# Kernel optimization log

Measured on AMD Instinct MI355X. Metric: run time of the kernel, lower is better.

## Reference

```python
import jax, jax.numpy as jnp
import numpy as np

B, T, C, H = 4, 2048, 768, 12
HD = C // H
EPS = 1e-5

def _ln(x, s, b):
    m = jnp.mean(x, axis=-1, keepdims=True)
    v = jnp.mean(jnp.square(x - m), axis=-1, keepdims=True)
    return (x - m) * jax.lax.rsqrt(v + EPS) * s + b

def setup_inputs() -> dict:
    key = jax.random.key(0)
    ks = jax.random.split(key, 8)
    x = jax.random.normal(ks[0], (B, T, C), dtype=jnp.float32)
    mask = jnp.tril(jnp.ones((T, T), dtype=bool))[None, None, :, :]  # causal [1,1,T,T]
    s = lambda fan_in: 1.0 / np.sqrt(fan_in)
    return {
        "x": x,
        "mask": mask,
        "ln1_s": jnp.ones((C,), jnp.float32),
        "ln1_b": jnp.zeros((C,), jnp.float32),
        "w_attn": jax.random.normal(ks[1], (C, 3 * C), jnp.float32) * s(C),
        "b_attn": jnp.zeros((3 * C,), jnp.float32),
        "w_o": jax.random.normal(ks[2], (C, C), jnp.float32) * s(C),
        "b_o": jnp.zeros((C,), jnp.float32),
        "ln2_s": jnp.ones((C,), jnp.float32),
        "ln2_b": jnp.zeros((C,), jnp.float32),
        "w_fc": jax.random.normal(ks[3], (C, 4 * C), jnp.float32) * s(C),
        "b_fc": jnp.zeros((4 * C,), jnp.float32),
        "w_proj": jax.random.normal(ks[4], (4 * C, C), jnp.float32) * s(4 * C),
        "b_proj": jnp.zeros((C,), jnp.float32),
    }

def reference(x, mask, ln1_s, ln1_b, w_attn, b_attn, w_o, b_o,
              ln2_s, ln2_b, w_fc, b_fc, w_proj, b_proj):
    # --- attention branch (pre-LN) ---
    h = _ln(x, ln1_s, ln1_b)
    qkv = (h @ w_attn + b_attn).reshape(B, T, 3 * H, HD)
    q, k, v = jnp.array_split(qkv, 3, axis=2)  # each [B,T,H,HD]
    scale = 1.0 / jnp.sqrt(jnp.float32(HD))
    attn = jnp.einsum('bqhd,bkhd->bhqk', q, k) * scale
    attn = jnp.where(mask, attn, jnp.finfo(jnp.float32).min)
    attn = jax.nn.softmax(attn, axis=-1)
    ctx = jnp.einsum('bhqk,bkhd->bqhd', attn, v).reshape(B, T, C)
    x = x + ctx @ w_o + b_o
    # --- MLP branch (pre-LN) ---
    h = _ln(x, ln2_s, ln2_b)
    h = jax.nn.gelu(h @ w_fc + b_fc, approximate=True)
    x = x + h @ w_proj + b_proj
    return x
```

## Files before the change

### kernel.cpp

```cpp
#include <hip/hip_runtime.h>


typedef unsigned short u16;
typedef unsigned int u32;
typedef __attribute__((ext_vector_type(8))) short short8;
typedef __attribute__((ext_vector_type(4))) float f32x4;
typedef __attribute__((ext_vector_type(16))) float f32x16;

__device__ __forceinline__ u16 f2bf(float f) {
    union { float f; unsigned u; } v; v.f = f;
    unsigned u = v.u;
    unsigned r = (u + 0x7FFFu + ((u >> 16) & 1u)) >> 16;
    return (u16)r;
}

__device__ __forceinline__ u32 cvtpk_bf16(float lo, float hi) {
    u32 r;
    asm("v_cvt_pk_bf16_f32 %0, %1, %2" : "=v"(r) : "v"(lo), "v"(hi));
    return r;
}

__device__ __forceinline__ void gld16(const u16* g, u16* l) {
    __builtin_amdgcn_global_load_lds(
        (const __attribute__((address_space(1))) void*)g,
        (__attribute__((address_space(3))) void*)l, 16, 0, 0);
}

__device__ __forceinline__ float gelu_fast(float v) {
    float t = v * v;
    float z2n = v * (-2.3022078f - 0.10294376f * t);
    float e = __builtin_amdgcn_exp2f(z2n);
    return v * __builtin_amdgcn_rcpf(1.0f + e);
}

__global__ void transpose_all_kernel(const float* __restrict__ w_attn, u16* __restrict__ wT_attn,
                                     const float* __restrict__ w_o,    u16* __restrict__ wT_o,
                                     const float* __restrict__ w_fc,   u16* __restrict__ wT_fc,
                                     const float* __restrict__ w_proj, u16* __restrict__ wT_proj) {
    __shared__ float t[32][33];
    int tile = blockIdx.x;
    const float* w; u16* wt; int N; int idx;
    if (tile < 1728)      { w = w_attn; wt = wT_attn; N = 2304; idx = tile; }
    else if (tile < 2304) { w = w_o;    wt = wT_o;    N = 768;  idx = tile - 1728; }
    else if (tile < 4608) { w = w_fc;   wt = wT_fc;   N = 3072; idx = tile - 2304; }
    else                  { w = w_proj; wt = wT_proj; N = 768;  idx = tile - 4608; }
    int K = (tile >= 4608) ? 3072 : 768;
    int nx = N / 32;
    int n0 = (idx % nx) * 32, k0 = (idx / nx) * 32;
    int tx = threadIdx.x, ty = threadIdx.y;
#pragma unroll
    for (int i = 0; i < 4; i++)
        t[ty + 8 * i][tx] = w[(size_t)(k0 + ty + 8 * i) * N + n0 + tx];
    __syncthreads();
#pragma unroll
    for (int i = 0; i < 4; i++)
        wt[(size_t)(n0 + ty + 8 * i) * K + k0 + tx] = f2bf(t[tx][ty + 8 * i]);
}

__global__ void ln_kernel(const float* __restrict__ x, const float* __restrict__ s,
                          const float* __restrict__ b, u16* __restrict__ out) {
    int row = blockIdx.x;
    int tid = threadIdx.x;
    const float* xr = x + (size_t)row * 768;
    float v0 = xr[tid], v1 = xr[tid + 256], v2 = xr[tid + 512];
    float sum = v0 + v1 + v2;
    float sq = v0 * v0 + v1 * v1 + v2 * v2;
#pragma unroll
    for (int off = 32; off; off >>= 1) {
        sum += __shfl_down(sum, off);
        sq += __shfl_down(sq, off);
    }
    __shared__ float red[8];
    int wid = tid >> 6, lane = tid & 63;
    if (lane == 0) { red[wid] = sum; red[4 + wid] = sq; }
    __syncthreads();
    if (tid == 0) {
        float s4 = red[0] + red[1] + red[2] + red[3];
        float q4 = red[4] + red[5] + red[6] + red[7];
        red[0] = s4 * (1.0f / 768.0f);
        red[1] = q4 * (1.0f / 768.0f);
    }
    __syncthreads();
    float mean = red[0];
    float var = red[1] - mean * mean;
    float rstd = rsqrtf(var + 1e-5f);
    u16* orow = out + (size_t)row * 768;
    orow[tid]       = f2bf((v0 - mean) * rstd * s[tid]       + b[tid]);
    orow[tid + 256] = f2bf((v1 - mean) * rstd * s[tid + 256] + b[tid + 256]);
    orow[tid + 512] = f2bf((v2 - mean) * rstd * s[tid + 512] + b[tid + 512]);
}

template <int GELU, int RES, int OUTMODE, int BM>
__global__ __launch_bounds__(256) void gemm_kernel(
    const u16* __restrict__ A, const u16* __restrict__ Wt,
    const float* __restrict__ bias, const float* __restrict__ res,
    void* __restrict__ out, int M, int N, int K,
    u16* __restrict__ qbuf, u16* __restrict__ kbuf, u16* __restrict__ vbuf) {
    constexpr int FM = BM / 32;
    constexpr int SA = BM / 32;
    constexpr int WR = BM / 2;
    __shared__ __align__(16) u16 lA[2][BM * 64];
    __shared__ __align__(16) u16 lB[2][128 * 64];
    int m0 = blockIdx.x * BM, n0 = blockIdx.y * 128;
    int tid = threadIdx.x;
    int wid = tid >> 6, lane = tid & 63;
    int wr = wid >> 1, wc = wid & 1;
    int l15 = lane & 15, lhi = lane >> 4;

    const u16* aptr[SA];
    const u16* bptr[4];
#pragma unroll
    for (int s = 0; s < SA; s++) {
        int u = s * 256 + tid;
        int row = u >> 3;
        int c8 = (u & 7) ^ (row & 7);
        aptr[s] = A + (size_t)(m0 + row) * K + c8 * 8;
    }
#pragma unroll
    for (int s = 0; s < 4; s++) {
        int u = s * 256 + tid;
        int row = u >> 3;
        int c8 = (u & 7) ^ (row & 7);
        bptr[s] = Wt + (size_t)(n0 + row) * K + c8 * 8;
    }

    f32x4 acc[FM][4];
#pragma unroll
    for (int i = 0; i < FM; i++)
#pragma unroll
        for (int j = 0; j < 4; j++) acc[i][j] = (f32x4)0.0f;

#pragma unroll
    for (int s = 0; s < SA; s++) gld16(aptr[s], &lA[0][(s * 256 + tid) * 8]);
#pragma unroll
    for (int s = 0; s < 4; s++) gld16(bptr[s], &lB[0][(s * 256 + tid) * 8]);
    __syncthreads();

    int KT = K >> 6;
    int cur = 0;
    for (int t = 0; t < KT; t++) {
        if (t + 1 < KT) {
            int ko = (t + 1) << 6;
#pragma unroll
            for (int s = 0; s < SA; s++) gld16(aptr[s] + ko, &lA[cur ^ 1][(s * 256 + tid) * 8]);
#pragma unroll
            for (int s = 0; s < 4; s++) gld16(bptr[s] + ko, &lB[cur ^ 1][(s * 256 + tid) * 8]);
        }
        short8 af[2][FM], bfr[2][4];
#pragma unroll
        for (int ks = 0; ks < 2; ks++) {
#pragma unroll
            for (int f = 0; f < FM; f++) {
                int ra = wr * WR + f * 16 + l15;
                af[ks][f] = *(const short8*)&lA[cur][ra * 64 + (((ks * 4 + lhi) ^ (ra & 7)) << 3)];
            }
#pragma unroll
            for (int f = 0; f < 4; f++) {
                int rb = wc * 64 + f * 16 + l15;
                bfr[ks][f] = *(const short8*)&lB[cur][rb * 64 + (((ks * 4 + lhi) ^ (rb & 7)) << 3)];
            }
        }
#pragma unroll
        for (int ks = 0; ks < 2; ks++)
#pragma unroll
            for (int fm = 0; fm < FM; fm++)
#pragma unroll
                for (int fn = 0; fn < 4; fn++)
                    acc[fm][fn] = __builtin_amdgcn_mfma_f32_16x16x32_bf16(
                        af[ks][fm], bfr[ks][fn], acc[fm][fn], 0, 0, 0);
        __syncthreads();
        cur ^= 1;
    }

    if (OUTMODE == 2) {
        int region = n0 / 768;
#pragma unroll
        for (int fm = 0; fm < FM; fm++)
#pragma unroll
            for (int fn = 0; fn < 4; fn++) {
                int col = n0 + wc * 64 + fn * 16 + l15;
                float bv = bias[col];
                int c = col - region * 768;
                int h = c >> 6, d = c & 63;
#pragma unroll
                for (int r = 0; r < 4; r++) {
                    int row = m0 + wr * WR + fm * 16 + lhi * 4 + r;
                    int bb = row >> 11, t = row & 2047;
                    u16 val = f2bf(acc[fm][fn][r] + bv);
                    size_t bh = (size_t)bb * 12 + h;
                    if (region == 0)      qbuf[(bh * 2048 + t) * 64 + d] = val;
                    else if (region == 1) kbuf[(bh * 2048 + t) * 64 + d] = val;
                    else                  vbuf[(bh * 64 + d) * 2048 + t] = val;
                }
            }
    } else {
#pragma unroll
        for (int fm = 0; fm < FM; fm++)
#pragma unroll
            for (int fn = 0; fn < 4; fn++) {
                int col = n0 + wc * 64 + fn * 16 + l15;
                float bv = bias[col];
#pragma unroll
                for (int r = 0; r < 4; r++) {
                    int row = m0 + wr * WR + fm * 16 + lhi * 4 + r;
                    float v = acc[fm][fn][r] + bv;
                    if (RES) v += res[(size_t)row * N + col];
                    if (GELU) v = gelu_fast(v);
                    if (OUTMODE == 1)
                        ((u16*)out)[(size_t)row * N + col] = f2bf(v);
                    else
                        ((float*)out)[(size_t)row * N + col] = v;
                }
            }
    }
}

__global__ __launch_bounds__(256) void attn_kernel(const u16* __restrict__ qbuf,
                                                   const u16* __restrict__ kbuf,
                                                   const u16* __restrict__ vbuf,
                                                   u16* __restrict__ ctx) {
    int bid = blockIdx.x;
    int qt = 15 - (bid / 48);
    int bh = bid % 48;
    int b = bh / 12, h = bh % 12;
    int q0 = qt * 128;
    int tid = threadIdx.x, wid = tid >> 6, lane = tid & 63;
    int l31 = lane & 31, hi = lane >> 5;

    __shared__ __align__(16) u16 lK[2][64 * 64];
    __shared__ __align__(16) u16 lV[2][64 * 64];

    const size_t bhT = (size_t)bh * 2048;

    const u16* kp[2];
    const u16* vp[2];
#pragma unroll
    for (int s = 0; s < 2; s++) {
        int u = s * 256 + tid;
        int row = u >> 3;
        int c8 = (u & 7) ^ (row & 7);
        kp[s] = kbuf + (bhT + row) * 64 + c8 * 8;
        vp[s] = vbuf + ((size_t)bh * 64 + row) * 2048 + c8 * 8;
    }

    int qrow = q0 + wid * 32 + l31;
    short8 bq[4];
#pragma unroll
    for (int ks = 0; ks < 4; ks++)
        bq[ks] = *(const short8*)(qbuf + (bhT + qrow) * 64 + ks * 16 + hi * 8);

    short8 ones;
#pragma unroll
    for (int j = 0; j < 8; j++) ones[j] = (short)0x3F80;

    f32x16 oacc[2], sacc;
#pragma unroll
    for (int dt = 0; dt < 2; dt++) oacc[dt] = (f32x16)0.0f;
    sacc = (f32x16)0.0f;
    float mb = -1e30f;
    const float C2 = 0.125f * 1.44269504089f;
    const float THR = 11.55f;
    int myq = q0 + wid * 32 + l31;
    int qmax = q0 + wid * 32 + 31;

    int nt = 2 * qt + 2;
#pragma unroll
    for (int s = 0; s < 2; s++) gld16(kp[s], &lK[0][(s * 256 + tid) * 8]);
#pragma unroll
    for (int s = 0; s < 2; s++) gld16(vp[s], &lV[0][(s * 256 + tid) * 8]);
    __syncthreads();

    int cur = 0;
    for (int t = 0; t < nt; t++) {
        int k0 = t * 64;
        if (t + 1 < nt) {
            int kn = (t + 1) * 64;
#pragma unroll
            for (int s = 0; s < 2; s++) gld16(kp[s] + (size_t)kn * 64, &lK[cur ^ 1][(s * 256 + tid) * 8]);
#pragma unroll
            for (int s = 0; s < 2; s++) gld16(vp[s] + kn, &lV[cur ^ 1][(s * 256 + tid) * 8]);
        }
        if (k0 <= qmax) {
            f32x16 sa[2];
#pragma unroll
            for (int kt = 0; kt < 2; kt++) sa[kt] = (f32x16)0.0f;
            __builtin_amdgcn_s_setprio(1);
#pragma unroll
            for (int kt = 0; kt < 2; kt++) {
                int rk = kt * 32 + l31;
#pragma unroll
                for (int ks = 0; ks < 4; ks++) {
                    short8 ak = *(const short8*)&lK[cur][rk * 64 + (((ks * 2 + hi) ^ (rk & 7)) << 3)];
                    sa[kt] = __builtin_amdgcn_mfma_f32_32x32x16_bf16(ak, bq[ks], sa[kt], 0, 0, 0);
                }
            }
            __builtin_amdgcn_s_setprio(0);
            if (k0 + 63 > q0 + wid * 32) {
#pragma unroll
                for (int kt = 0; kt < 2; kt++)
#pragma unroll
                    for (int r = 0; r < 16; r++) {
                        int key = k0 + kt * 32 + (r & 3) + 8 * (r >> 2) + 4 * hi;
                        if (key > myq) sa[kt][r] = -1e30f;
                    }
            }
            float tmax = -1e30f;
#pragma unroll
            for (int kt = 0; kt < 2; kt++)
#pragma unroll
                for (int r = 0; r < 16; r += 2)
                    tmax = fmaxf(tmax, fmaxf(sa[kt][r], sa[kt][r + 1]));
            tmax = fmaxf(tmax, __shfl_xor(tmax, 32));
            float tmb = tmax * C2;
            if (__any(tmb > mb + THR)) {
                float mbn = fmaxf(mb, tmb);
                float corr = __builtin_amdgcn_exp2f(mb - mbn);
#pragma unroll
                for (int r = 0; r < 16; r++) {
                    int qm = (r & 3) + 8 * (r >> 2) + 4 * hi;
                    float c = __shfl(corr, qm);
                    oacc[0][r] *= c;
                    oacc[1][r] *= c;
                    sacc[r] *= c;
                }
                mb = mbn;
            }
#pragma unroll
            for (int kt = 0; kt < 2; kt++)
#pragma unroll
                for (int r = 0; r < 16; r++)
                    sa[kt][r] = __builtin_amdgcn_exp2f(fmaf(sa[kt][r], C2, -mb));
            short8 pa[4];
#pragma unroll
            for (int kt = 0; kt < 2; kt++)
#pragma unroll
                for (int ks2 = 0; ks2 < 2; ks2++) {
                    int base = ks2 * 8;
                    u32 A0 = cvtpk_bf16(sa[kt][base + 0], sa[kt][base + 1]);
                    u32 B0 = cvtpk_bf16(sa[kt][base + 4], sa[kt][base + 5]);
                    u32 A1 = cvtpk_bf16(sa[kt][base + 2], sa[kt][base + 3]);
                    u32 B1 = cvtpk_bf16(sa[kt][base + 6], sa[kt][base + 7]);
                    u32 A0s = (u32)__shfl_xor((int)A0, 32);
                    u32 B0s = (u32)__shfl_xor((int)B0, 32);
                    u32 A1s = (u32)__shfl_xor((int)A1, 32);
                    u32 B1s = (u32)__shfl_xor((int)B1, 32);
                    union { u32 u[4]; short8 s; } w;
                    w.u[0] = hi ? B0s : A0;
                    w.u[1] = hi ? B1s : A1;
                    w.u[2] = hi ? B0 : A0s;
                    w.u[3] = hi ? B1 : A1s;
                    pa[kt * 2 + ks2] = w.s;
                }
            __builtin_amdgcn_s_setprio(1);
#pragma unroll
            for (int kt = 0; kt < 2; kt++)
#pragma unroll
                for (int ks2 = 0; ks2 < 2; ks2++) {
                    short8 ap = pa[kt * 2 + ks2];
#pragma unroll
                    for (int dt = 0; dt < 2; dt++) {
                        int rd = dt * 32 + l31;
                        short8 bv = *(const short8*)&lV[cur][rd * 64 + (((kt * 4 + ks2 * 2 + hi) ^ (rd & 7)) << 3)];
                        oacc[dt] = __builtin_amdgcn_mfma_f32_32x32x16_bf16(ap, bv, oacc[dt], 0, 0, 0);
                    }
                    sacc = __builtin_amdgcn_mfma_f32_32x32x16_bf16(ap, ones, sacc, 0, 0, 0);
                }
            __builtin_amdgcn_s_setprio(0);
        }
        __syncthreads();
        cur ^= 1;
    }
    const size_t rowb = (size_t)b * 2048;
#pragma unroll
    for (int r = 0; r < 16; r++) {
        float ir = __builtin_amdgcn_rcpf(sacc[r]);
        int qm = (r & 3) + 8 * (r >> 2) + 4 * hi;
        int row = q0 + wid * 32 + qm;
        u16* op = ctx + (rowb + row) * 768 + h * 64 + l31;
        op[0]  = f2bf(oacc[0][r] * ir);
        op[32] = f2bf(oacc[1][r] * ir);
    }
}

extern "C" void kernel_launch(void* const* d_in, const int* in_sizes, int n_in,
                              void* d_out, int out_size, void* d_ws, size_t ws_size,
                              hipStream_t stream) {
    const float* x      = (const float*)d_in[0];
    const float* ln1_s  = (const float*)d_in[2];
    const float* ln1_b  = (const float*)d_in[3];
    const float* w_attn = (const float*)d_in[4];
    const float* b_attn = (const float*)d_in[5];
    const float* w_o    = (const float*)d_in[6];
    const float* b_o    = (const float*)d_in[7];
    const float* ln2_s  = (const float*)d_in[8];
    const float* ln2_b  = (const float*)d_in[9];
    const float* w_fc   = (const float*)d_in[10];
    const float* b_fc   = (const float*)d_in[11];
    const float* w_proj = (const float*)d_in[12];
    const float* b_proj = (const float*)d_in[13];

    char* ws = (char*)d_ws;
    u16* wT_attn = (u16*)(ws + 0);
    u16* wT_o    = (u16*)(ws + 3538944);
    u16* wT_fc   = (u16*)(ws + 4718592);
    u16* wT_proj = (u16*)(ws + 9437184);
    u16* bufA    = (u16*)(ws + 14155776);
    u16* qbuf    = (u16*)(ws + 26738688);
    u16* kbuf    = (u16*)(ws + 39321600);
    u16* vbuf    = (u16*)(ws + 51904512);
    u16* act     = (u16*)(ws + 26738688);
    float* x1    = (float*)(ws + 77070336);

    transpose_all_kernel<<<6912, dim3(32, 8), 0, stream>>>(w_attn, wT_attn, w_o, wT_o,
                                                           w_fc, wT_fc, w_proj, wT_proj);

    ln_kernel<<<8192, 256, 0, stream>>>(x, ln1_s, ln1_b, bufA);
    gemm_kernel<0, 0, 2, 128><<<dim3(64, 18), 256, 0, stream>>>(bufA, wT_attn, b_attn, nullptr, nullptr,
                                                                8192, 2304, 768, qbuf, kbuf, vbuf);
    attn_kernel<<<768, 256, 0, stream>>>(qbuf, kbuf, vbuf, bufA);
    gemm_kernel<0, 1, 0, 64><<<dim3(128, 6), 256, 0, stream>>>(bufA, wT_o, b_o, x, x1,
                                                               8192, 768, 768, nullptr, nullptr, nullptr);
    ln_kernel<<<8192, 256, 0, stream>>>(x1, ln2_s, ln2_b, bufA);
    gemm_kernel<1, 0, 1, 128><<<dim3(64, 24), 256, 0, stream>>>(bufA, wT_fc, b_fc, nullptr, act,
                                                                8192, 3072, 768, nullptr, nullptr, nullptr);
    gemm_kernel<0, 1, 0, 64><<<dim3(128, 6), 256, 0, stream>>>(act, wT_proj, b_proj, x1, (float*)d_out,
                                                               8192, 768, 3072, nullptr, nullptr, nullptr);
}
```

Measured before the change: 267.8 us.

## Split GEMM into 256-row big-tile kernel and single-buffered small kernel

```diff
diff --git a/kernel.cpp b/kernel.cpp
--- a/kernel.cpp
+++ b/kernel.cpp
@@ -90,92 +90,73 @@
     orow[tid + 512] = f2bf((v2 - mean) * rstd * s[tid + 512] + b[tid + 512]);
 }
 
-template <int GELU, int RES, int OUTMODE, int BM>
-__global__ __launch_bounds__(256) void gemm_kernel(
+template <int GELU, int OUTMODE>
+__global__ __launch_bounds__(512) void gemm_big_kernel(
     const u16* __restrict__ A, const u16* __restrict__ Wt,
-    const float* __restrict__ bias, const float* __restrict__ res,
-    void* __restrict__ out, int M, int N, int K,
+    const float* __restrict__ bias, void* __restrict__ out,
+    int M, int N, int K,
     u16* __restrict__ qbuf, u16* __restrict__ kbuf, u16* __restrict__ vbuf) {
-    constexpr int FM = BM / 32;
-    constexpr int SA = BM / 32;
-    constexpr int WR = BM / 2;
-    __shared__ __align__(16) u16 lA[2][BM * 64];
-    __shared__ __align__(16) u16 lB[2][128 * 64];
-    int m0 = blockIdx.x * BM, n0 = blockIdx.y * 128;
+    __shared__ __align__(16) u16 lA[256 * 64];
+    __shared__ __align__(16) u16 lB[128 * 64];
+    int m0 = blockIdx.x * 256, n0 = blockIdx.y * 128;
     int tid = threadIdx.x;
     int wid = tid >> 6, lane = tid & 63;
     int wr = wid >> 1, wc = wid & 1;
     int l15 = lane & 15, lhi = lane >> 4;
 
-    const u16* aptr[SA];
-    const u16* bptr[4];
-#pragma unroll
-    for (int s = 0; s < SA; s++) {
-        int u = s * 256 + tid;
+    const u16* aptr[4];
+    const u16* bptr[2];
+#pragma unroll
+    for (int s = 0; s < 4; s++) {
+        int u = s * 512 + tid;
         int row = u >> 3;
         int c8 = (u & 7) ^ (row & 7);
         aptr[s] = A + (size_t)(m0 + row) * K + c8 * 8;
     }
 #pragma unroll
-    for (int s = 0; s < 4; s++) {
-        int u = s * 256 + tid;
+    for (int s = 0; s < 2; s++) {
+        int u = s * 512 + tid;
         int row = u >> 3;
         int c8 = (u & 7) ^ (row & 7);
         bptr[s] = Wt + (size_t)(n0 + row) * K + c8 * 8;
     }
 
-    f32x4 acc[FM][4];
-#pragma unroll
-    for (int i = 0; i < FM; i++)
+    f32x4 acc[4][4];
+#pragma unroll
+    for (int i = 0; i < 4; i++)
 #pragma unroll
         for (int j = 0; j < 4; j++) acc[i][j] = (f32x4)0.0f;
 
-#pragma unroll
-    for (int s = 0; s < SA; s++) gld16(aptr[s], &lA[0][(s * 256 + tid) * 8]);
-#pragma unroll
-    for (int s = 0; s < 4; s++) gld16(bptr[s], &lB[0][(s * 256 + tid) * 8]);
-    __syncthreads();
-
-    int KT = K >> 6;
-    int cur = 0;
-    for (int t = 0; t < KT; t++) {
-        if (t + 1 < KT) {
-            int ko = (t + 1) << 6;
-#pragma unroll
-            for (int s = 0; s < SA; s++) gld16(aptr[s] + ko, &lA[cur ^ 1][(s * 256 + tid) * 8]);
-#pragma unroll
-            for (int s = 0; s < 4; s++) gld16(bptr[s] + ko, &lB[cur ^ 1][(s * 256 + tid) * 8]);
-        }
-        short8 af[2][FM], bfr[2][4];
+    for (int k0 = 0; k0 < K; k0 += 64) {
+#pragma unroll
+        for (int s = 0; s < 4; s++) gld16(aptr[s] + k0, &lA[(s * 512 + tid) * 8]);
+#pragma unroll
+        for (int s = 0; s < 2; s++) gld16(bptr[s] + k0, &lB[(s * 512 + tid) * 8]);
+        __syncthreads();
 #pragma unroll
         for (int ks = 0; ks < 2; ks++) {
-#pragma unroll
-            for (int f = 0; f < FM; f++) {
-                int ra = wr * WR + f * 16 + l15;
-                af[ks][f] = *(const short8*)&lA[cur][ra * 64 + (((ks * 4 + lhi) ^ (ra & 7)) << 3)];
-            }
+            short8 af[4], bfr[4];
 #pragma unroll
             for (int f = 0; f < 4; f++) {
+                int ra = wr * 64 + f * 16 + l15;
+                af[f] = *(const short8*)&lA[ra * 64 + (((ks * 4 + lhi) ^ (ra & 7)) << 3)];
                 int rb = wc * 64 + f * 16 + l15;
-                bfr[ks][f] = *(const short8*)&lB[cur][rb * 64 + (((ks * 4 + lhi) ^ (rb & 7)) << 3)];
-            }
-        }
-#pragma unroll
-        for (int ks = 0; ks < 2; ks++)
-#pragma unroll
-            for (int fm = 0; fm < FM; fm++)
+                bfr[f] = *(const short8*)&lB[rb * 64 + (((ks * 4 + lhi) ^ (rb & 7)) << 3)];
+            }
+#pragma unroll
+            for (int fm = 0; fm < 4; fm++)
 #pragma unroll
                 for (int fn = 0; fn < 4; fn++)
                     acc[fm][fn] = __builtin_amdgcn_mfma_f32_16x16x32_bf16(
-                        af[ks][fm], bfr[ks][fn], acc[fm][fn], 0, 0, 0);
+                        af[fm], bfr[fn], acc[fm][fn], 0, 0, 0);
+        }
         __syncthreads();
-        cur ^= 1;
     }
 
     if (OUTMODE == 2) {
         int region = n0 / 768;
 #pragma unroll
-        for (int fm = 0; fm < FM; fm++)
+        for (int fm = 0; fm < 4; fm++)
 #pragma unroll
             for (int fn = 0; fn < 4; fn++) {
                 int col = n0 + wc * 64 + fn * 16 + l15;
@@ -184,7 +165,7 @@
                 int h = c >> 6, d = c & 63;
 #pragma unroll
                 for (int r = 0; r < 4; r++) {
-                    int row = m0 + wr * WR + fm * 16 + lhi * 4 + r;
+                    int row = m0 + wr * 64 + fm * 16 + lhi * 4 + r;
                     int bb = row >> 11, t = row & 2047;
                     u16 val = f2bf(acc[fm][fn][r] + bv);
                     size_t bh = (size_t)bb * 12 + h;
@@ -195,24 +176,97 @@
             }
     } else {
 #pragma unroll
-        for (int fm = 0; fm < FM; fm++)
+        for (int fm = 0; fm < 4; fm++)
 #pragma unroll
             for (int fn = 0; fn < 4; fn++) {
                 int col = n0 + wc * 64 + fn * 16 + l15;
                 float bv = bias[col];
 #pragma unroll
                 for (int r = 0; r < 4; r++) {
-                    int row = m0 + wr * WR + fm * 16 + lhi * 4 + r;
+                    int row = m0 + wr * 64 + fm * 16 + lhi * 4 + r;
                     float v = acc[fm][fn][r] + bv;
-                    if (RES) v += res[(size_t)row * N + col];
                     if (GELU) v = gelu_fast(v);
-                    if (OUTMODE == 1)
-                        ((u16*)out)[(size_t)row * N + col] = f2bf(v);
-                    else
-                        ((float*)out)[(size_t)row * N + col] = v;
-                }
-            }
-    }
+                    ((u16*)out)[(size_t)row * N + col] = f2bf(v);
+                }
+            }
+    }
+}
+
+__global__ __launch_bounds__(256) void gemm_small_kernel(
+    const u16* __restrict__ A, const u16* __restrict__ Wt,
+    const float* __restrict__ bias, const float* __restrict__ res,
+    float* __restrict__ out, int M, int N, int K) {
+    __shared__ __align__(16) u16 lA[64 * 64];
+    __shared__ __align__(16) u16 lB[128 * 64];
+    int m0 = blockIdx.x * 64, n0 = blockIdx.y * 128;
+    int tid = threadIdx.x;
+    int wid = tid >> 6, lane = tid & 63;
+    int wr = wid >> 1, wc = wid & 1;
+    int l15 = lane & 15, lhi = lane >> 4;
+
+    const u16* aptr[2];
+    const u16* bptr[4];
+#pragma unroll
+    for (int s = 0; s < 2; s++) {
+        int u = s * 256 + tid;
+        int row = u >> 3;
+        int c8 = (u & 7) ^ (row & 7);
+        aptr[s] = A + (size_t)(m0 + row) * K + c8 * 8;
+    }
+#pragma unroll
+    for (int s = 0; s < 4; s++) {
+        int u = s * 256 + tid;
+        int row = u >> 3;
+        int c8 = (u & 7) ^ (row & 7);
+        bptr[s] = Wt + (size_t)(n0 + row) * K + c8 * 8;
+    }
+
+    f32x4 acc[2][4];
+#pragma unroll
+    for (int i = 0; i < 2; i++)
+#pragma unroll
+        for (int j = 0; j < 4; j++) acc[i][j] = (f32x4)0.0f;
+
+    for (int k0 = 0; k0 < K; k0 += 64) {
+#pragma unroll
+        for (int s = 0; s < 2; s++) gld16(aptr[s] + k0, &lA[(s * 256 + tid) * 8]);
+#pragma unroll
+        for (int s = 0; s < 4; s++) gld16(bptr[s] + k0, &lB[(s * 256 + tid) * 8]);
+        __syncthreads();
+#pragma unroll
+        for (int ks = 0; ks < 2; ks++) {
+            short8 af[2], bfr[4];
+#pragma unroll
+            for (int f = 0; f < 2; f++) {
+                int ra = wr * 32 + f * 16 + l15;
+                af[f] = *(const short8*)&lA[ra * 64 + (((ks * 4 + lhi) ^ (ra & 7)) << 3)];
+            }
+#pragma unroll
+            for (int f = 0; f < 4; f++) {
+                int rb = wc * 64 + f * 16 + l15;
+                bfr[f] = *(const short8*)&lB[rb * 64 + (((ks * 4 + lhi) ^ (rb & 7)) << 3)];
+            }
+#pragma unroll
+            for (int fm = 0; fm < 2; fm++)
+#pragma unroll
+                for (int fn = 0; fn < 4; fn++)
+                    acc[fm][fn] = __builtin_amdgcn_mfma_f32_16x16x32_bf16(
+                        af[fm], bfr[fn], acc[fm][fn], 0, 0, 0);
+        }
+        __syncthreads();
+    }
+#pragma unroll
+    for (int fm = 0; fm < 2; fm++)
+#pragma unroll
+        for (int fn = 0; fn < 4; fn++) {
+            int col = n0 + wc * 64 + fn * 16 + l15;
+            float bv = bias[col];
+#pragma unroll
+            for (int r = 0; r < 4; r++) {
+                int row = m0 + wr * 32 + fm * 16 + lhi * 4 + r;
+                out[(size_t)row * N + col] = acc[fm][fn][r] + bv + res[(size_t)row * N + col];
+            }
+        }
 }
 
 __global__ __launch_bounds__(256) void attn_kernel(const u16* __restrict__ qbuf,
@@ -415,14 +469,13 @@
                                                            w_fc, wT_fc, w_proj, wT_proj);
 
     ln_kernel<<<8192, 256, 0, stream>>>(x, ln1_s, ln1_b, bufA);
-    gemm_kernel<0, 0, 2, 128><<<dim3(64, 18), 256, 0, stream>>>(bufA, wT_attn, b_attn, nullptr, nullptr,
-                                                                8192, 2304, 768, qbuf, kbuf, vbuf);
+    gemm_big_kernel<0, 2><<<dim3(32, 18), 512, 0, stream>>>(bufA, wT_attn, b_attn, nullptr,
+                                                            8192, 2304, 768, qbuf, kbuf, vbuf);
     attn_kernel<<<768, 256, 0, stream>>>(qbuf, kbuf, vbuf, bufA);
-    gemm_kernel<0, 1, 0, 64><<<dim3(128, 6), 256, 0, stream>>>(bufA, wT_o, b_o, x, x1,
-                                                               8192, 768, 768, nullptr, nullptr, nullptr);
+    gemm_small_kernel<<<dim3(128, 6), 256, 0, stream>>>(bufA, wT_o, b_o, x, x1, 8192, 768, 768);
     ln_kernel<<<8192, 256, 0, stream>>>(x1, ln2_s, ln2_b, bufA);
-    gemm_kernel<1, 0, 1, 128><<<dim3(64, 24), 256, 0, stream>>>(bufA, wT_fc, b_fc, nullptr, act,
-                                                                8192, 3072, 768, nullptr, nullptr, nullptr);
-    gemm_kernel<0, 1, 0, 64><<<dim3(128, 6), 256, 0, stream>>>(act, wT_proj, b_proj, x1, (float*)d_out,
-                                                               8192, 768, 3072, nullptr, nullptr, nullptr);
-}
+    gemm_big_kernel<1, 1><<<dim3(32, 24), 512, 0, stream>>>(bufA, wT_fc, b_fc, act,
+                                                            8192, 3072, 768, nullptr, nullptr, nullptr);
+    gemm_small_kernel<<<dim3(128, 6), 256, 0, stream>>>(act, wT_proj, b_proj, x1, (float*)d_out,
+                                                        8192, 768, 3072);
+}
```

Measured after the change: 258.4 us. 3.5% less time.

## Prefetch GEMM tiles two stages ahead with explicit vmcnt waits and priority

Applied to the files above, without the earlier changes.

```diff
diff --git a/kernel.cpp b/kernel.cpp
--- a/kernel.cpp
+++ b/kernel.cpp
@@ -90,92 +90,87 @@
     orow[tid + 512] = f2bf((v2 - mean) * rstd * s[tid + 512] + b[tid + 512]);
 }
 
-template <int GELU, int RES, int OUTMODE, int BM>
+template <int GELU, int RES, int OUTMODE>
 __global__ __launch_bounds__(256) void gemm_kernel(
     const u16* __restrict__ A, const u16* __restrict__ Wt,
     const float* __restrict__ bias, const float* __restrict__ res,
     void* __restrict__ out, int M, int N, int K,
     u16* __restrict__ qbuf, u16* __restrict__ kbuf, u16* __restrict__ vbuf) {
-    constexpr int FM = BM / 32;
-    constexpr int SA = BM / 32;
-    constexpr int WR = BM / 2;
-    __shared__ __align__(16) u16 lA[2][BM * 64];
+    __shared__ __align__(16) u16 lA[2][128 * 64];
     __shared__ __align__(16) u16 lB[2][128 * 64];
-    int m0 = blockIdx.x * BM, n0 = blockIdx.y * 128;
+    int m0 = blockIdx.x * 128, n0 = blockIdx.y * 128;
     int tid = threadIdx.x;
     int wid = tid >> 6, lane = tid & 63;
     int wr = wid >> 1, wc = wid & 1;
     int l15 = lane & 15, lhi = lane >> 4;
 
-    const u16* aptr[SA];
+    const u16* aptr[4];
     const u16* bptr[4];
 #pragma unroll
-    for (int s = 0; s < SA; s++) {
+    for (int s = 0; s < 4; s++) {
         int u = s * 256 + tid;
         int row = u >> 3;
         int c8 = (u & 7) ^ (row & 7);
         aptr[s] = A + (size_t)(m0 + row) * K + c8 * 8;
-    }
-#pragma unroll
-    for (int s = 0; s < 4; s++) {
-        int u = s * 256 + tid;
-        int row = u >> 3;
-        int c8 = (u & 7) ^ (row & 7);
         bptr[s] = Wt + (size_t)(n0 + row) * K + c8 * 8;
     }
 
-    f32x4 acc[FM][4];
-#pragma unroll
-    for (int i = 0; i < FM; i++)
+    auto stage = [&](int t, int buf) {
+        int ko = t << 6;
+#pragma unroll
+        for (int s = 0; s < 4; s++) gld16(aptr[s] + ko, &lA[buf][(s * 256 + tid) * 8]);
+#pragma unroll
+        for (int s = 0; s < 4; s++) gld16(bptr[s] + ko, &lB[buf][(s * 256 + tid) * 8]);
+    };
+
+    f32x4 acc[4][4];
+#pragma unroll
+    for (int i = 0; i < 4; i++)
 #pragma unroll
         for (int j = 0; j < 4; j++) acc[i][j] = (f32x4)0.0f;
 
-#pragma unroll
-    for (int s = 0; s < SA; s++) gld16(aptr[s], &lA[0][(s * 256 + tid) * 8]);
-#pragma unroll
-    for (int s = 0; s < 4; s++) gld16(bptr[s], &lB[0][(s * 256 + tid) * 8]);
-    __syncthreads();
-
     int KT = K >> 6;
+    stage(0, 0);
+    stage(1, 1);
+
     int cur = 0;
     for (int t = 0; t < KT; t++) {
-        if (t + 1 < KT) {
-            int ko = (t + 1) << 6;
-#pragma unroll
-            for (int s = 0; s < SA; s++) gld16(aptr[s] + ko, &lA[cur ^ 1][(s * 256 + tid) * 8]);
-#pragma unroll
-            for (int s = 0; s < 4; s++) gld16(bptr[s] + ko, &lB[cur ^ 1][(s * 256 + tid) * 8]);
-        }
-        short8 af[2][FM], bfr[2][4];
-#pragma unroll
-        for (int ks = 0; ks < 2; ks++) {
-#pragma unroll
-            for (int f = 0; f < FM; f++) {
-                int ra = wr * WR + f * 16 + l15;
+        if (t + 1 < KT) asm volatile("s_waitcnt vmcnt(8)" ::: "memory");
+        else            asm volatile("s_waitcnt vmcnt(0)" ::: "memory");
+        __builtin_amdgcn_s_barrier();
+        __builtin_amdgcn_sched_barrier(0);
+
+        short8 af[2][4], bfr[2][4];
+#pragma unroll
+        for (int ks = 0; ks < 2; ks++)
+#pragma unroll
+            for (int f = 0; f < 4; f++) {
+                int ra = wr * 64 + f * 16 + l15;
                 af[ks][f] = *(const short8*)&lA[cur][ra * 64 + (((ks * 4 + lhi) ^ (ra & 7)) << 3)];
-            }
-#pragma unroll
-            for (int f = 0; f < 4; f++) {
                 int rb = wc * 64 + f * 16 + l15;
                 bfr[ks][f] = *(const short8*)&lB[cur][rb * 64 + (((ks * 4 + lhi) ^ (rb & 7)) << 3)];
             }
-        }
+        __builtin_amdgcn_s_setprio(1);
 #pragma unroll
         for (int ks = 0; ks < 2; ks++)
 #pragma unroll
-            for (int fm = 0; fm < FM; fm++)
+            for (int fm = 0; fm < 4; fm++)
 #pragma unroll
                 for (int fn = 0; fn < 4; fn++)
                     acc[fm][fn] = __builtin_amdgcn_mfma_f32_16x16x32_bf16(
                         af[ks][fm], bfr[ks][fn], acc[fm][fn], 0, 0, 0);
-        __syncthreads();
+        __builtin_amdgcn_s_setprio(0);
+        __builtin_amdgcn_sched_barrier(0);
+        __builtin_amdgcn_s_barrier();
+        __builtin_amdgcn_sched_barrier(0);
+        if (t + 2 < KT) stage(t + 2, cur);
         cur ^= 1;
     }
 
     if (OUTMODE == 2) {
         int region = n0 / 768;
 #pragma unroll
-        for (int fm = 0; fm < FM; fm++)
+        for (int fm = 0; fm < 4; fm++)
 #pragma unroll
             for (int fn = 0; fn < 4; fn++) {
                 int col = n0 + wc * 64 + fn * 16 + l15;
@@ -184,7 +179,7 @@
                 int h = c >> 6, d = c & 63;
 #pragma unroll
                 for (int r = 0; r < 4; r++) {
-                    int row = m0 + wr * WR + fm * 16 + lhi * 4 + r;
+                    int row = m0 + wr * 64 + fm * 16 + lhi * 4 + r;
                     int bb = row >> 11, t = row & 2047;
                     u16 val = f2bf(acc[fm][fn][r] + bv);
                     size_t bh = (size_t)bb * 12 + h;
@@ -195,14 +190,14 @@
             }
     } else {
 #pragma unroll
-        for (int fm = 0; fm < FM; fm++)
+        for (int fm = 0; fm < 4; fm++)
 #pragma unroll
             for (int fn = 0; fn < 4; fn++) {
                 int col = n0 + wc * 64 + fn * 16 + l15;
                 float bv = bias[col];
 #pragma unroll
                 for (int r = 0; r < 4; r++) {
-                    int row = m0 + wr * WR + fm * 16 + lhi * 4 + r;
+                    int row = m0 + wr * 64 + fm * 16 + lhi * 4 + r;
                     float v = acc[fm][fn][r] + bv;
                     if (RES) v += res[(size_t)row * N + col];
                     if (GELU) v = gelu_fast(v);
@@ -415,14 +410,14 @@
                                                            w_fc, wT_fc, w_proj, wT_proj);
 
     ln_kernel<<<8192, 256, 0, stream>>>(x, ln1_s, ln1_b, bufA);
-    gemm_kernel<0, 0, 2, 128><<<dim3(64, 18), 256, 0, stream>>>(bufA, wT_attn, b_attn, nullptr, nullptr,
-                                                                8192, 2304, 768, qbuf, kbuf, vbuf);
+    gemm_kernel<0, 0, 2><<<dim3(64, 18), 256, 0, stream>>>(bufA, wT_attn, b_attn, nullptr, nullptr,
+                                                           8192, 2304, 768, qbuf, kbuf, vbuf);
     attn_kernel<<<768, 256, 0, stream>>>(qbuf, kbuf, vbuf, bufA);
-    gemm_kernel<0, 1, 0, 64><<<dim3(128, 6), 256, 0, stream>>>(bufA, wT_o, b_o, x, x1,
-                                                               8192, 768, 768, nullptr, nullptr, nullptr);
+    gemm_kernel<0, 1, 0><<<dim3(64, 6), 256, 0, stream>>>(bufA, wT_o, b_o, x, x1,
+                                                          8192, 768, 768, nullptr, nullptr, nullptr);
     ln_kernel<<<8192, 256, 0, stream>>>(x1, ln2_s, ln2_b, bufA);
-    gemm_kernel<1, 0, 1, 128><<<dim3(64, 24), 256, 0, stream>>>(bufA, wT_fc, b_fc, nullptr, act,
-                                                                8192, 3072, 768, nullptr, nullptr, nullptr);
-    gemm_kernel<0, 1, 0, 64><<<dim3(128, 6), 256, 0, stream>>>(act, wT_proj, b_proj, x1, (float*)d_out,
-                                                               8192, 768, 3072, nullptr, nullptr, nullptr);
-}
+    gemm_kernel<1, 0, 1><<<dim3(64, 24), 256, 0, stream>>>(bufA, wT_fc, b_fc, nullptr, act,
+                                                           8192, 3072, 768, nullptr, nullptr, nullptr);
+    gemm_kernel<0, 1, 0><<<dim3(64, 6), 256, 0, stream>>>(act, wT_proj, b_proj, x1, (float*)d_out,
+                                                          8192, 768, 3072, nullptr, nullptr, nullptr);
+}
```

Measured after the change: 268.5 us. Within noise of the previous version (+0.3%).
